# Performance work log

Hardware: AMD Instinct MI355X
Metric: run time of the kernel (lower is better)

The kernel has to match this reference:

```python
import jax, jax.numpy as jnp
import numpy as np

N_NODES = 65536
N_EDGES = 1048576
VOCAB = 50000
HIDDEN = 256
LAYERS = 3
NUM_GRAPHS = 64
NEG_SLOPE = 0.2  # PyG GATConv default LeakyReLU slope
EPS = 1e-16      # PyG softmax denominator epsilon


def setup_inputs() -> dict:
    key = jax.random.key(0)
    ks = jax.random.split(key, 12)
    s = 0.02
    nodes = jax.random.randint(ks[0], (N_NODES,), 0, VOCAB, dtype=jnp.int32)
    edge_index = jax.random.randint(ks[1], (2, N_EDGES), 0, N_NODES, dtype=jnp.int32)
    batch = jnp.sort(jax.random.randint(ks[2], (N_NODES,), 0, NUM_GRAPHS, dtype=jnp.int32))
    emb = jax.random.normal(ks[3], (VOCAB, HIDDEN), jnp.float32) * s
    Wg = jax.random.normal(ks[4], (LAYERS, HIDDEN, HIDDEN), jnp.float32) * s
    a_src = jax.random.normal(ks[5], (LAYERS, HIDDEN), jnp.float32) * s
    a_dst = jax.random.normal(ks[6], (LAYERS, HIDDEN), jnp.float32) * s
    bg = jnp.zeros((LAYERS, HIDDEN), jnp.float32)
    Wl = jax.random.normal(ks[7], (LAYERS, HIDDEN, HIDDEN), jnp.float32) * s
    bl = jnp.zeros((LAYERS, HIDDEN), jnp.float32)
    Wout = jax.random.normal(ks[8], (HIDDEN, VOCAB), jnp.float32) * s
    bout = jnp.zeros((VOCAB,), jnp.float32)
    return {"nodes": nodes, "edge_index": edge_index, "batch": batch,
            "emb": emb, "Wg": Wg, "a_src": a_src, "a_dst": a_dst, "bg": bg,
            "Wl": Wl, "bl": bl, "Wout": Wout, "bout": bout}


def _gat_layer(x, src, dst, W, a_s, a_d, b, n):
    h = x @ W                                    # [N, H]
    e = jax.nn.leaky_relu((h @ a_s)[src] + (h @ a_d)[dst], NEG_SLOPE)  # [E]
    m = jax.ops.segment_max(e, dst, num_segments=n)
    w = jnp.exp(e - m[dst])
    denom = jax.ops.segment_sum(w, dst, num_segments=n)
    alpha = w / (denom[dst] + EPS)               # segment softmax over incoming edges
    out = jax.ops.segment_sum(h[src] * alpha[:, None], dst, num_segments=n)
    return out + b


def reference(nodes, edge_index, batch, emb, Wg, a_src, a_dst, bg, Wl, bl, Wout, bout):
    n = nodes.shape[0]
    loop = jnp.arange(n, dtype=edge_index.dtype)  # GATConv add_self_loops=True
    src = jnp.concatenate([edge_index[0], loop])
    dst = jnp.concatenate([edge_index[1], loop])
    x = emb[nodes]                                # [N, H]
    for l in range(Wg.shape[0]):
        x = _gat_layer(x, src, dst, Wg[l], a_src[l], a_dst[l], bg[l], n)
        x = jax.nn.relu(x)
        x = x @ Wl[l] + bl[l]
    sums = jax.ops.segment_sum(x, batch, num_segments=NUM_GRAPHS)
    cnt = jax.ops.segment_sum(jnp.ones((n,), x.dtype), batch, num_segments=NUM_GRAPHS)
    pooled = sums / jnp.maximum(cnt, 1.0)[:, None]  # global mean pool -> [G, H]
    return pooled @ Wout + bout                      # [G, V]
```

## Files before the change

### kernel.cpp

```cpp
#include <hip/hip_runtime.h>

#define N_NODES 65536
#define N_EDGES 1048576
#define E_TOTAL (N_EDGES + N_NODES)
#define VOCAB 50000
#define HIDDEN 256
#define NUM_GRAPHS 64
#define NEG_SLOPE 0.2f
#define SM_EPS 1e-16f

#define NBKT 128
#define BKT_SHIFT 9
#define DSTS_PER_BKT 512
#define BKT_CAP 10240
#define EDGES_PER_BLK1 4352

typedef _Float16 f16x8 __attribute__((ext_vector_type(8)));
typedef _Float16 f16x4 __attribute__((ext_vector_type(4)));
typedef float f32x4 __attribute__((ext_vector_type(4)));

__global__ __launch_bounds__(256) void gather_kernel(const int* __restrict__ nodes,
    const float* __restrict__ emb, _Float16* __restrict__ x) {
    int i = blockIdx.x;
    int t = threadIdx.x;
    x[(size_t)i * HIDDEN + t] = (_Float16)emb[(size_t)nodes[i] * HIDDEN + t];
}

__global__ __launch_bounds__(256) void convert_wt_kernel(const float* __restrict__ Wg,
    _Float16* __restrict__ WT) {
    int n = blockIdx.x;
    int k = threadIdx.x;
    WT[(size_t)n * HIDDEN + k] = (_Float16)Wg[(size_t)k * HIDDEN + n];
}

__global__ __launch_bounds__(256) void fuse_w_kernel(const float* __restrict__ Wl,
    const float* __restrict__ Wg, _Float16* __restrict__ WT) {
    int pair = blockIdx.y;
    int n = blockIdx.x;
    int k = threadIdx.x;
    const float* A = Wl + (size_t)pair * HIDDEN * HIDDEN;
    const float* B = Wg + (size_t)(pair + 1) * HIDDEN * HIDDEN;
    float s = 0.f;
    for (int j = 0; j < HIDDEN; j++) s += A[(size_t)k * HIDDEN + j] * B[(size_t)j * HIDDEN + n];
    WT[(size_t)(1 + pair) * HIDDEN * HIDDEN + (size_t)n * HIDDEN + k] = (_Float16)s;
}

__global__ __launch_bounds__(256) void fuse_b_kernel(const float* __restrict__ Wg,
    const float* __restrict__ bl, float* __restrict__ bfused) {
    int pair = blockIdx.x;
    int n = threadIdx.x;
    const float* B = Wg + (size_t)(pair + 1) * HIDDEN * HIDDEN;
    const float* b = bl + (size_t)pair * HIDDEN;
    float s = 0.f;
    for (int k = 0; k < HIDDEN; k++) s += b[k] * B[(size_t)k * HIDDEN + n];
    bfused[pair * HIDDEN + n] = s;
}

__global__ __launch_bounds__(256) void bucket_kernel(const int* __restrict__ ei,
    int* __restrict__ bcur, unsigned* __restrict__ staging) {
    __shared__ int lhist[NBKT];
    __shared__ int lbase[NBKT];
    __shared__ int lcur[NBKT];
    int tid = threadIdx.x;
    if (tid < NBKT) lhist[tid] = 0;
    __syncthreads();
    int e0 = blockIdx.x * EDGES_PER_BLK1;
    int mySrc[17], myDst[17];
    #pragma unroll
    for (int k = 0; k < 17; k++) {
        int e = e0 + k * 256 + tid;
        int src, dst;
        if (e < N_EDGES) { src = ei[e]; dst = ei[N_EDGES + e]; }
        else             { src = dst = e - N_EDGES; }
        mySrc[k] = src; myDst[k] = dst;
        atomicAdd(&lhist[dst >> BKT_SHIFT], 1);
    }
    __syncthreads();
    if (tid < NBKT) {
        int c = lhist[tid];
        lbase[tid] = (c > 0) ? atomicAdd(&bcur[tid], c) : 0;
        lcur[tid] = 0;
    }
    __syncthreads();
    #pragma unroll
    for (int k = 0; k < 17; k++) {
        int b = myDst[k] >> BKT_SHIFT;
        int pos = lbase[b] + atomicAdd(&lcur[b], 1);
        staging[(size_t)b * BKT_CAP + pos] =
            ((unsigned)(myDst[k] & (DSTS_PER_BKT - 1)) << 16) | (unsigned)mySrc[k];
    }
}

__global__ __launch_bounds__(256) void csr_kernel(const int* __restrict__ bcur,
    const unsigned* __restrict__ staging, int* __restrict__ row_ptr,
    int* __restrict__ src_sorted) {
    __shared__ unsigned sedge[BKT_CAP];
    __shared__ int shist[DSTS_PER_BKT];
    __shared__ int sbase[DSTS_PER_BKT];
    __shared__ int spart[256];
    int b = blockIdx.x;
    int tid = threadIdx.x;
    int cnt = bcur[b];

    spart[tid] = (tid < NBKT && tid < b) ? bcur[tid] : 0;
    __syncthreads();
    for (int d = 128; d > 0; d >>= 1) {
        if (tid < d) spart[tid] += spart[tid + d];
        __syncthreads();
    }
    int base = spart[0];
    __syncthreads();

    shist[tid] = 0; shist[tid + 256] = 0;
    __syncthreads();
    for (int i = tid; i < cnt; i += 256) {
        unsigned v = staging[(size_t)b * BKT_CAP + i];
        sedge[i] = v;
        atomicAdd(&shist[v >> 16], 1);
    }
    __syncthreads();
    int p = shist[2 * tid] + shist[2 * tid + 1];
    spart[tid] = p;
    __syncthreads();
    for (int d = 1; d < 256; d <<= 1) {
        int v = (tid >= d) ? spart[tid - d] : 0;
        __syncthreads();
        spart[tid] += v;
        __syncthreads();
    }
    int epair = spart[tid] - p;
    sbase[2 * tid] = epair;
    sbase[2 * tid + 1] = epair + shist[2 * tid];
    __syncthreads();
    row_ptr[b * DSTS_PER_BKT + tid] = base + sbase[tid];
    row_ptr[b * DSTS_PER_BKT + 256 + tid] = base + sbase[256 + tid];
    shist[tid] = sbase[tid];
    shist[tid + 256] = sbase[tid + 256];
    __syncthreads();
    for (int i = tid; i < cnt; i += 256) {
        unsigned v = sedge[i];
        int d = v >> 16;
        int pos = atomicAdd(&shist[d], 1);
        src_sorted[base + pos] = (int)(v & 0xFFFFu);
    }
    if (b == NBKT - 1 && tid == 0) row_ptr[N_NODES] = E_TOTAL;
}

#define PAD_K 40
template <bool FUSED>
__global__ __launch_bounds__(256) void gemm_f16_kernel(const _Float16* __restrict__ A,
    const _Float16* __restrict__ WT, const float* __restrict__ bias,
    _Float16* __restrict__ C,
    const float* __restrict__ a_s, const float* __restrict__ a_d,
    float* __restrict__ es, float* __restrict__ ed) {
    __shared__ _Float16 As[128][PAD_K];
    __shared__ _Float16 Bs[128][PAD_K];
    int tid = threadIdx.x;
    int wave = tid >> 6;
    int lane = tid & 63;
    int quad = lane >> 4;
    int l16 = lane & 15;
    int m0 = blockIdx.x * 128;
    int n0 = blockIdx.y * 128;

    f32x4 acc[2][8];
    #pragma unroll
    for (int rt = 0; rt < 2; rt++)
        #pragma unroll
        for (int ct = 0; ct < 8; ct++)
            acc[rt][ct] = (f32x4){0.f, 0.f, 0.f, 0.f};

    for (int k0 = 0; k0 < HIDDEN; k0 += 32) {
        __syncthreads();
        #pragma unroll
        for (int i = 0; i < 2; i++) {
            int c = tid + i * 256;
            int row = c >> 2, q = c & 3;
            *(f16x8*)&As[row][q * 8] =
                *(const f16x8*)(A + (size_t)(m0 + row) * HIDDEN + k0 + q * 8);
        }
        #pragma unroll
        for (int i = 0; i < 2; i++) {
            int c = tid + i * 256;
            int row = c >> 2, q = c & 3;
            *(f16x8*)&Bs[row][q * 8] =
                *(const f16x8*)(WT + (size_t)(n0 + row) * HIDDEN + k0 + q * 8);
        }
        __syncthreads();
        f16x8 a0 = *(const f16x8*)&As[wave * 32 + l16][quad * 8];
        f16x8 a1 = *(const f16x8*)&As[wave * 32 + 16 + l16][quad * 8];
        #pragma unroll
        for (int ct = 0; ct < 8; ct++) {
            f16x8 b = *(const f16x8*)&Bs[ct * 16 + l16][quad * 8];
            acc[0][ct] = __builtin_amdgcn_mfma_f32_16x16x32_f16(a0, b, acc[0][ct], 0, 0, 0);
            acc[1][ct] = __builtin_amdgcn_mfma_f32_16x16x32_f16(a1, b, acc[1][ct], 0, 0, 0);
        }
    }
    #pragma unroll
    for (int rt = 0; rt < 2; rt++) {
        #pragma unroll
        for (int ct = 0; ct < 8; ct++) {
            int col = n0 + ct * 16 + l16;
            float bv = (bias != nullptr) ? bias[col] : 0.f;
            int rowbase = m0 + wave * 32 + rt * 16 + quad * 4;
            #pragma unroll
            for (int r = 0; r < 4; r++) {
                float hv = acc[rt][ct][r] + bv;
                acc[rt][ct][r] = hv;
                C[(size_t)(rowbase + r) * HIDDEN + col] = (_Float16)hv;
            }
        }
    }
    if (FUSED) {
        #pragma unroll
        for (int rt = 0; rt < 2; rt++) {
            float ds0 = 0.f, ds1 = 0.f, ds2 = 0.f, ds3 = 0.f;
            float dd0 = 0.f, dd1 = 0.f, dd2 = 0.f, dd3 = 0.f;
            #pragma unroll
            for (int ct = 0; ct < 8; ct++) {
                int col = n0 + ct * 16 + l16;
                float av = a_s[col];
                float dv = a_d[col];
                ds0 += acc[rt][ct][0] * av; dd0 += acc[rt][ct][0] * dv;
                ds1 += acc[rt][ct][1] * av; dd1 += acc[rt][ct][1] * dv;
                ds2 += acc[rt][ct][2] * av; dd2 += acc[rt][ct][2] * dv;
                ds3 += acc[rt][ct][3] * av; dd3 += acc[rt][ct][3] * dv;
            }
            #pragma unroll
            for (int off = 1; off < 16; off <<= 1) {
                ds0 += __shfl_xor(ds0, off); dd0 += __shfl_xor(dd0, off);
                ds1 += __shfl_xor(ds1, off); dd1 += __shfl_xor(dd1, off);
                ds2 += __shfl_xor(ds2, off); dd2 += __shfl_xor(dd2, off);
                ds3 += __shfl_xor(ds3, off); dd3 += __shfl_xor(dd3, off);
            }
            if (l16 == 0) {
                int rowbase = m0 + wave * 32 + rt * 16 + quad * 4;
                atomicAdd(&es[rowbase + 0], ds0); atomicAdd(&ed[rowbase + 0], dd0);
                atomicAdd(&es[rowbase + 1], ds1); atomicAdd(&ed[rowbase + 1], dd1);
                atomicAdd(&es[rowbase + 2], ds2); atomicAdd(&ed[rowbase + 2], dd2);
                atomicAdd(&es[rowbase + 3], ds3); atomicAdd(&ed[rowbase + 3], dd3);
            }
        }
    }
}

__global__ __launch_bounds__(256) void agg_kernel(const _Float16* __restrict__ h,
    const int* __restrict__ row_ptr, const int* __restrict__ src_sorted,
    const float* __restrict__ es, const float* __restrict__ ed,
    const float* __restrict__ bg, _Float16* __restrict__ g) {
    int dst = blockIdx.x * 8 + (threadIdx.x >> 5);
    int l32 = threadIdx.x & 31;
    int start = row_ptr[dst];
    int end = row_ptr[dst + 1];
    float edd = ed[dst];
    const _Float16* hl = h + l32 * 8;

    float den0 = 0.f, den1 = 0.f;
    float acc[8];
    #pragma unroll
    for (int j = 0; j < 8; j++) acc[j] = 0.f;

    int i = start;
    for (; i + 7 < end; i += 8) {
        int s0 = src_sorted[i + 0];
        int s1 = src_sorted[i + 1];
        int s2 = src_sorted[i + 2];
        int s3 = src_sorted[i + 3];
        int s4 = src_sorted[i + 4];
        int s5 = src_sorted[i + 5];
        int s6 = src_sorted[i + 6];
        int s7 = src_sorted[i + 7];
        f16x8 r0 = *(const f16x8*)(hl + (unsigned)s0 * HIDDEN);
        f16x8 r1 = *(const f16x8*)(hl + (unsigned)s1 * HIDDEN);
        f16x8 r2 = *(const f16x8*)(hl + (unsigned)s2 * HIDDEN);
        f16x8 r3 = *(const f16x8*)(hl + (unsigned)s3 * HIDDEN);
        f16x8 r4 = *(const f16x8*)(hl + (unsigned)s4 * HIDDEN);
        f16x8 r5 = *(const f16x8*)(hl + (unsigned)s5 * HIDDEN);
        f16x8 r6 = *(const f16x8*)(hl + (unsigned)s6 * HIDDEN);
        f16x8 r7 = *(const f16x8*)(hl + (unsigned)s7 * HIDDEN);
        float e0 = es[s0] + edd; e0 = (e0 > 0.f) ? e0 : NEG_SLOPE * e0;
        float e1 = es[s1] + edd; e1 = (e1 > 0.f) ? e1 : NEG_SLOPE * e1;
        float e2 = es[s2] + edd; e2 = (e2 > 0.f) ? e2 : NEG_SLOPE * e2;
        float e3 = es[s3] + edd; e3 = (e3 > 0.f) ? e3 : NEG_SLOPE * e3;
        float e4 = es[s4] + edd; e4 = (e4 > 0.f) ? e4 : NEG_SLOPE * e4;
        float e5 = es[s5] + edd; e5 = (e5 > 0.f) ? e5 : NEG_SLOPE * e5;
        float e6 = es[s6] + edd; e6 = (e6 > 0.f) ? e6 : NEG_SLOPE * e6;
        float e7 = es[s7] + edd; e7 = (e7 > 0.f) ? e7 : NEG_SLOPE * e7;
        float w0 = __expf(e0);
        float w1 = __expf(e1);
        float w2 = __expf(e2);
        float w3 = __expf(e3);
        float w4 = __expf(e4);
        float w5 = __expf(e5);
        float w6 = __expf(e6);
        float w7 = __expf(e7);
        den0 += (w0 + w1) + (w2 + w3);
        den1 += (w4 + w5) + (w6 + w7);
        #pragma unroll
        for (int j = 0; j < 8; j++)
            acc[j] += (w0 * (float)r0[j] + w1 * (float)r1[j])
                    + (w2 * (float)r2[j] + w3 * (float)r3[j])
                    + (w4 * (float)r4[j] + w5 * (float)r5[j])
                    + (w6 * (float)r6[j] + w7 * (float)r7[j]);
    }
    for (; i + 3 < end; i += 4) {
        int s0 = src_sorted[i + 0];
        int s1 = src_sorted[i + 1];
        int s2 = src_sorted[i + 2];
        int s3 = src_sorted[i + 3];
        f16x8 r0 = *(const f16x8*)(hl + (unsigned)s0 * HIDDEN);
        f16x8 r1 = *(const f16x8*)(hl + (unsigned)s1 * HIDDEN);
        f16x8 r2 = *(const f16x8*)(hl + (unsigned)s2 * HIDDEN);
        f16x8 r3 = *(const f16x8*)(hl + (unsigned)s3 * HIDDEN);
        float e0 = es[s0] + edd; e0 = (e0 > 0.f) ? e0 : NEG_SLOPE * e0;
        float e1 = es[s1] + edd; e1 = (e1 > 0.f) ? e1 : NEG_SLOPE * e1;
        float e2 = es[s2] + edd; e2 = (e2 > 0.f) ? e2 : NEG_SLOPE * e2;
        float e3 = es[s3] + edd; e3 = (e3 > 0.f) ? e3 : NEG_SLOPE * e3;
        float w0 = __expf(e0);
        float w1 = __expf(e1);
        float w2 = __expf(e2);
        float w3 = __expf(e3);
        den0 += (w0 + w1) + (w2 + w3);
        #pragma unroll
        for (int j = 0; j < 8; j++)
            acc[j] += (w0 * (float)r0[j] + w1 * (float)r1[j])
                    + (w2 * (float)r2[j] + w3 * (float)r3[j]);
    }
    for (; i < end; i++) {
        int s0 = src_sorted[i];
        f16x8 r0 = *(const f16x8*)(hl + (unsigned)s0 * HIDDEN);
        float e0 = es[s0] + edd; e0 = (e0 > 0.f) ? e0 : NEG_SLOPE * e0;
        float w0 = __expf(e0);
        den1 += w0;
        #pragma unroll
        for (int j = 0; j < 8; j++) acc[j] += w0 * (float)r0[j];
    }

    float inv = 1.0f / ((den0 + den1) + SM_EPS);
    float4 b0 = *(const float4*)(bg + l32 * 8);
    float4 b1 = *(const float4*)(bg + l32 * 8 + 4);
    f16x8 outv;
    outv[0] = (_Float16)fmaxf(acc[0] * inv + b0.x, 0.f);
    outv[1] = (_Float16)fmaxf(acc[1] * inv + b0.y, 0.f);
    outv[2] = (_Float16)fmaxf(acc[2] * inv + b0.z, 0.f);
    outv[3] = (_Float16)fmaxf(acc[3] * inv + b0.w, 0.f);
    outv[4] = (_Float16)fmaxf(acc[4] * inv + b1.x, 0.f);
    outv[5] = (_Float16)fmaxf(acc[5] * inv + b1.y, 0.f);
    outv[6] = (_Float16)fmaxf(acc[6] * inv + b1.z, 0.f);
    outv[7] = (_Float16)fmaxf(acc[7] * inv + b1.w, 0.f);
    *(f16x8*)(g + (size_t)dst * HIDDEN + l32 * 8) = outv;
}

__global__ __launch_bounds__(128) void graph_bounds_kernel(const int* __restrict__ batch,
    int* __restrict__ gstart) {
    int g = threadIdx.x;
    if (g > NUM_GRAPHS) return;
    if (g == NUM_GRAPHS) { gstart[NUM_GRAPHS] = N_NODES; return; }
    int lo = 0, hi = N_NODES;
    while (lo < hi) {
        int mid = (lo + hi) >> 1;
        if (batch[mid] < g) lo = mid + 1; else hi = mid;
    }
    gstart[g] = lo;
}

#define POOL_SPLITS 16
__global__ __launch_bounds__(256) void pool_partial_kernel(const _Float16* __restrict__ x,
    const int* __restrict__ gstart, float* __restrict__ pooledT) {
    int g = blockIdx.x;
    int chunk = blockIdx.y;
    int t = threadIdx.x;
    int s = gstart[g];
    int e = gstart[g + 1];
    int n = e - s;
    int per = (n + POOL_SPLITS - 1) / POOL_SPLITS;
    int r0 = s + chunk * per;
    int r1 = min(r0 + per, e);
    if (r0 >= r1) return;
    float acc = 0.f;
    for (int r = r0; r < r1; r++) acc += (float)x[(size_t)r * HIDDEN + t];
    atomicAdd(&pooledT[t * NUM_GRAPHS + g], acc);
}

__global__ __launch_bounds__(256) void mean_kernel(const float* __restrict__ pooledT,
    const int* __restrict__ gstart, float* __restrict__ meanT) {
    int i = blockIdx.x * 256 + threadIdx.x;
    int g = i & (NUM_GRAPHS - 1);
    float c = (float)max(gstart[g + 1] - gstart[g], 1);
    meanT[i] = pooledT[i] / c;
}

__global__ __launch_bounds__(256) void wl2_kernel(const float* __restrict__ meanP,
    const float* __restrict__ Wl, const float* __restrict__ bl,
    float* __restrict__ meanT2) {
    int g = blockIdx.x;
    int n = threadIdx.x;
    const float* W2 = Wl + (size_t)2 * HIDDEN * HIDDEN;
    float s = bl[2 * HIDDEN + n];
    for (int k = 0; k < HIDDEN; k++)
        s += meanP[k * NUM_GRAPHS + g] * W2[(size_t)k * HIDDEN + n];
    meanT2[n * NUM_GRAPHS + g] = s;
}

__global__ __launch_bounds__(256) void final_kernel(const float* __restrict__ meanT,
    const float* __restrict__ Wout, const float* __restrict__ bout, float* __restrict__ out) {
    int j = blockIdx.x * 64 + (threadIdx.x & 63);
    int g0 = __builtin_amdgcn_readfirstlane((threadIdx.x >> 6) * 16);
    if (j >= VOCAB) return;
    float acc[16];
    #pragma unroll
    for (int g = 0; g < 16; g++) acc[g] = 0.f;
    #pragma unroll 4
    for (int k = 0; k < HIDDEN; k++) {
        float w = Wout[(size_t)k * VOCAB + j];
        const float* mrow = meanT + k * NUM_GRAPHS + g0;
        #pragma unroll
        for (int g = 0; g < 16; g++) acc[g] += mrow[g] * w;
    }
    float b = bout[j];
    #pragma unroll
    for (int g = 0; g < 16; g++) out[(size_t)(g0 + g) * VOCAB + j] = acc[g] + b;
}

extern "C" void kernel_launch(void* const* d_in, const int* in_sizes, int n_in,
                              void* d_out, int out_size, void* d_ws, size_t ws_size,
                              hipStream_t stream) {
    const int*   nodes = (const int*)d_in[0];
    const int*   ei    = (const int*)d_in[1];
    const int*   batch = (const int*)d_in[2];
    const float* emb   = (const float*)d_in[3];
    const float* Wg    = (const float*)d_in[4];
    const float* a_src = (const float*)d_in[5];
    const float* a_dst = (const float*)d_in[6];
    const float* bg    = (const float*)d_in[7];
    const float* Wl    = (const float*)d_in[8];
    const float* bl    = (const float*)d_in[9];
    const float* Wout  = (const float*)d_in[10];
    const float* bout  = (const float*)d_in[11];
    float* out = (float*)d_out;

    char* ws = (char*)d_ws;
    size_t off = 0;
    auto alloc = [&](size_t bytes) -> void* {
        void* p = ws + off;
        off += (bytes + 255) & ~(size_t)255;
        return p;
    };
    _Float16* bufA    = (_Float16*)alloc((size_t)N_NODES * HIDDEN * 2);
    _Float16* bufB    = (_Float16*)alloc((size_t)N_NODES * HIDDEN * 2);
    _Float16* WT      = (_Float16*)alloc((size_t)3 * HIDDEN * HIDDEN * 2);
    float* bfused     = (float*)alloc((size_t)2 * HIDDEN * 4);
    float* es         = (float*)alloc((size_t)N_NODES * 4);
    float* ed         = (float*)alloc((size_t)N_NODES * 4);
    int*   row_ptr    = (int*)alloc((size_t)(N_NODES + 1) * 4);
    int*   src_sorted = (int*)alloc((size_t)E_TOTAL * 4);
    int*   bcur       = (int*)alloc((size_t)NBKT * 4);
    unsigned* staging = (unsigned*)alloc((size_t)NBKT * BKT_CAP * 4);
    float* pooledT    = (float*)alloc((size_t)HIDDEN * NUM_GRAPHS * 4);
    float* meanT      = (float*)alloc((size_t)HIDDEN * NUM_GRAPHS * 4);
    float* meanT2     = (float*)alloc((size_t)HIDDEN * NUM_GRAPHS * 4);
    int*   gstart     = (int*)alloc((size_t)(NUM_GRAPHS + 1) * 4);

    hipMemsetAsync(bcur, 0, (size_t)NBKT * 4, stream);
    hipMemsetAsync(pooledT, 0, (size_t)HIDDEN * NUM_GRAPHS * 4, stream);

    convert_wt_kernel<<<HIDDEN, 256, 0, stream>>>(Wg, WT);
    fuse_w_kernel<<<dim3(HIDDEN, 2), 256, 0, stream>>>(Wl, Wg, WT);
    fuse_b_kernel<<<2, 256, 0, stream>>>(Wg, bl, bfused);
    gather_kernel<<<N_NODES, 256, 0, stream>>>(nodes, emb, bufA);
    bucket_kernel<<<E_TOTAL / EDGES_PER_BLK1, 256, 0, stream>>>(ei, bcur, staging);
    csr_kernel<<<NBKT, 256, 0, stream>>>(bcur, staging, row_ptr, src_sorted);

    for (int l = 0; l < 3; l++) {
        hipMemsetAsync(es, 0, (size_t)N_NODES * 4, stream);
        hipMemsetAsync(ed, 0, (size_t)N_NODES * 4, stream);
        const float* bias = (l == 0) ? nullptr : (bfused + (size_t)(l - 1) * HIDDEN);
        gemm_f16_kernel<true><<<dim3(N_NODES / 128, 2), 256, 0, stream>>>(
            bufA, WT + (size_t)l * HIDDEN * HIDDEN, bias, bufB,
            a_src + (size_t)l * HIDDEN, a_dst + (size_t)l * HIDDEN, es, ed);
        agg_kernel<<<N_NODES / 8, 256, 0, stream>>>(
            bufB, row_ptr, src_sorted, es, ed, bg + (size_t)l * HIDDEN, bufA);
    }

    graph_bounds_kernel<<<1, 128, 0, stream>>>(batch, gstart);
    pool_partial_kernel<<<dim3(NUM_GRAPHS, POOL_SPLITS), 256, 0, stream>>>(bufA, gstart, pooledT);
    mean_kernel<<<(HIDDEN * NUM_GRAPHS) / 256, 256, 0, stream>>>(pooledT, gstart, meanT);
    wl2_kernel<<<NUM_GRAPHS, 256, 0, stream>>>(meanT, Wl, bl, meanT2);
    final_kernel<<<dim3((VOCAB + 63) / 64), 256, 0, stream>>>(meanT2, Wout, bout, out);
}
```

Measured before the change: 694.1 us.

## Sort destinations by degree for aggregation and replace atomics with partial-sum buffers

Measured after the change: 695.9 us. Within noise of the previous version (+0.3%).

```diff
diff --git a/kernel.cpp b/kernel.cpp
--- a/kernel.cpp
+++ b/kernel.cpp
@@ -14,6 +14,7 @@
 #define DSTS_PER_BKT 512
 #define BKT_CAP 10240
 #define EDGES_PER_BLK1 4352
+#define DEGBINS 128
 
 typedef _Float16 f16x8 __attribute__((ext_vector_type(8)));
 typedef _Float16 f16x4 __attribute__((ext_vector_type(4)));
@@ -146,13 +147,61 @@
     if (b == NBKT - 1 && tid == 0) row_ptr[N_NODES] = E_TOTAL;
 }
 
+__global__ __launch_bounds__(256) void deghist_kernel(const int* __restrict__ row_ptr,
+    int* __restrict__ dhist) {
+    __shared__ int lh[DEGBINS];
+    int tid = threadIdx.x;
+    if (tid < DEGBINS) lh[tid] = 0;
+    __syncthreads();
+    int d = blockIdx.x * 256 + tid;
+    int deg = min(row_ptr[d + 1] - row_ptr[d], DEGBINS - 1);
+    atomicAdd(&lh[deg], 1);
+    __syncthreads();
+    if (tid < DEGBINS && lh[tid]) atomicAdd(&dhist[tid], lh[tid]);
+}
+
+__global__ __launch_bounds__(128) void degscan_kernel(const int* __restrict__ dhist,
+    int* __restrict__ dbase) {
+    __shared__ int s[DEGBINS];
+    int t = threadIdx.x;
+    s[t] = dhist[t];
+    __syncthreads();
+    for (int d = 1; d < DEGBINS; d <<= 1) {
+        int v = (t >= d) ? s[t - d] : 0;
+        __syncthreads();
+        s[t] += v;
+        __syncthreads();
+    }
+    dbase[t] = s[t] - dhist[t];
+}
+
+__global__ __launch_bounds__(256) void degscatter_kernel(const int* __restrict__ row_ptr,
+    int* __restrict__ dbase, int* __restrict__ perm) {
+    __shared__ int lh[DEGBINS], lb[DEGBINS], lc[DEGBINS];
+    int tid = threadIdx.x;
+    if (tid < DEGBINS) lh[tid] = 0;
+    __syncthreads();
+    int d = blockIdx.x * 256 + tid;
+    int deg = min(row_ptr[d + 1] - row_ptr[d], DEGBINS - 1);
+    atomicAdd(&lh[deg], 1);
+    __syncthreads();
+    if (tid < DEGBINS) {
+        int c = lh[tid];
+        lb[tid] = c ? atomicAdd(&dbase[tid], c) : 0;
+        lc[tid] = 0;
+    }
+    __syncthreads();
+    int pos = lb[deg] + atomicAdd(&lc[deg], 1);
+    perm[pos] = d;
+}
+
 #define PAD_K 40
 template <bool FUSED>
 __global__ __launch_bounds__(256) void gemm_f16_kernel(const _Float16* __restrict__ A,
     const _Float16* __restrict__ WT, const float* __restrict__ bias,
     _Float16* __restrict__ C,
     const float* __restrict__ a_s, const float* __restrict__ a_d,
-    float* __restrict__ es, float* __restrict__ ed) {
+    float* __restrict__ esp, float* __restrict__ edp) {
     __shared__ _Float16 As[128][PAD_K];
     __shared__ _Float16 Bs[128][PAD_K];
     int tid = threadIdx.x;
@@ -212,6 +261,8 @@
         }
     }
     if (FUSED) {
+        float* esb = esp + (size_t)blockIdx.y * N_NODES;
+        float* edb = edp + (size_t)blockIdx.y * N_NODES;
         #pragma unroll
         for (int rt = 0; rt < 2; rt++) {
             float ds0 = 0.f, ds1 = 0.f, ds2 = 0.f, ds3 = 0.f;
@@ -235,20 +286,28 @@
             }
             if (l16 == 0) {
                 int rowbase = m0 + wave * 32 + rt * 16 + quad * 4;
-                atomicAdd(&es[rowbase + 0], ds0); atomicAdd(&ed[rowbase + 0], dd0);
-                atomicAdd(&es[rowbase + 1], ds1); atomicAdd(&ed[rowbase + 1], dd1);
-                atomicAdd(&es[rowbase + 2], ds2); atomicAdd(&ed[rowbase + 2], dd2);
-                atomicAdd(&es[rowbase + 3], ds3); atomicAdd(&ed[rowbase + 3], dd3);
+                esb[rowbase + 0] = ds0; edb[rowbase + 0] = dd0;
+                esb[rowbase + 1] = ds1; edb[rowbase + 1] = dd1;
+                esb[rowbase + 2] = ds2; edb[rowbase + 2] = dd2;
+                esb[rowbase + 3] = ds3; edb[rowbase + 3] = dd3;
             }
         }
     }
 }
 
+__global__ __launch_bounds__(256) void combine_kernel(const float* __restrict__ esp,
+    const float* __restrict__ edp, float* __restrict__ es, float* __restrict__ ed) {
+    int i = blockIdx.x * 256 + threadIdx.x;
+    es[i] = esp[i] + esp[N_NODES + i];
+    ed[i] = edp[i] + edp[N_NODES + i];
+}
+
 __global__ __launch_bounds__(256) void agg_kernel(const _Float16* __restrict__ h,
     const int* __restrict__ row_ptr, const int* __restrict__ src_sorted,
+    const int* __restrict__ perm,
     const float* __restrict__ es, const float* __restrict__ ed,
     const float* __restrict__ bg, _Float16* __restrict__ g) {
-    int dst = blockIdx.x * 8 + (threadIdx.x >> 5);
+    int dst = perm[blockIdx.x * 8 + (threadIdx.x >> 5)];
     int l32 = threadIdx.x & 31;
     int start = row_ptr[dst];
     int end = row_ptr[dst + 1];
@@ -450,11 +509,16 @@
     _Float16* bufB    = (_Float16*)alloc((size_t)N_NODES * HIDDEN * 2);
     _Float16* WT      = (_Float16*)alloc((size_t)3 * HIDDEN * HIDDEN * 2);
     float* bfused     = (float*)alloc((size_t)2 * HIDDEN * 4);
+    float* esp        = (float*)alloc((size_t)2 * N_NODES * 4);
+    float* edp        = (float*)alloc((size_t)2 * N_NODES * 4);
     float* es         = (float*)alloc((size_t)N_NODES * 4);
     float* ed         = (float*)alloc((size_t)N_NODES * 4);
     int*   row_ptr    = (int*)alloc((size_t)(N_NODES + 1) * 4);
     int*   src_sorted = (int*)alloc((size_t)E_TOTAL * 4);
+    int*   perm       = (int*)alloc((size_t)N_NODES * 4);
     int*   bcur       = (int*)alloc((size_t)NBKT * 4);
+    int*   dhist      = (int*)alloc((size_t)DEGBINS * 4);
+    int*   dbase      = (int*)alloc((size_t)DEGBINS * 4);
     unsigned* staging = (unsigned*)alloc((size_t)NBKT * BKT_CAP * 4);
     float* pooledT    = (float*)alloc((size_t)HIDDEN * NUM_GRAPHS * 4);
     float* meanT      = (float*)alloc((size_t)HIDDEN * NUM_GRAPHS * 4);
@@ -462,6 +526,7 @@
     int*   gstart     = (int*)alloc((size_t)(NUM_GRAPHS + 1) * 4);
 
     hipMemsetAsync(bcur, 0, (size_t)NBKT * 4, stream);
+    hipMemsetAsync(dhist, 0, (size_t)DEGBINS * 4, stream);
     hipMemsetAsync(pooledT, 0, (size_t)HIDDEN * NUM_GRAPHS * 4, stream);
 
     convert_wt_kernel<<<HIDDEN, 256, 0, stream>>>(Wg, WT);
@@ -470,16 +535,18 @@
     gather_kernel<<<N_NODES, 256, 0, stream>>>(nodes, emb, bufA);
     bucket_kernel<<<E_TOTAL / EDGES_PER_BLK1, 256, 0, stream>>>(ei, bcur, staging);
     csr_kernel<<<NBKT, 256, 0, stream>>>(bcur, staging, row_ptr, src_sorted);
+    deghist_kernel<<<N_NODES / 256, 256, 0, stream>>>(row_ptr, dhist);
+    degscan_kernel<<<1, DEGBINS, 0, stream>>>(dhist, dbase);
+    degscatter_kernel<<<N_NODES / 256, 256, 0, stream>>>(row_ptr, dbase, perm);
 
     for (int l = 0; l < 3; l++) {
-        hipMemsetAsync(es, 0, (size_t)N_NODES * 4, stream);
-        hipMemsetAsync(ed, 0, (size_t)N_NODES * 4, stream);
         const float* bias = (l == 0) ? nullptr : (bfused + (size_t)(l - 1) * HIDDEN);
         gemm_f16_kernel<true><<<dim3(N_NODES / 128, 2), 256, 0, stream>>>(
             bufA, WT + (size_t)l * HIDDEN * HIDDEN, bias, bufB,
-            a_src + (size_t)l * HIDDEN, a_dst + (size_t)l * HIDDEN, es, ed);
+            a_src + (size_t)l * HIDDEN, a_dst + (size_t)l * HIDDEN, esp, edp);
+        combine_kernel<<<N_NODES / 256, 256, 0, stream>>>(esp, edp, es, ed);
         agg_kernel<<<N_NODES / 8, 256, 0, stream>>>(
-            bufB, row_ptr, src_sorted, es, ed, bg + (size_t)l * HIDDEN, bufA);
+            bufB, row_ptr, src_sorted, perm, es, ed, bg + (size_t)l * HIDDEN, bufA);
     }
 
     graph_bounds_kernel<<<1, 128, 0, stream>>>(batch, gstart);
```

## Use full-width GEMM tiles so attention logits are stored without atomics

Applied to the files above, without the earlier changes.

After: 675.8 us. 2.6% less time.

```diff
diff --git a/kernel.cpp b/kernel.cpp
--- a/kernel.cpp
+++ b/kernel.cpp
@@ -26,23 +26,22 @@
     x[(size_t)i * HIDDEN + t] = (_Float16)emb[(size_t)nodes[i] * HIDDEN + t];
 }
 
-__global__ __launch_bounds__(256) void convert_wt_kernel(const float* __restrict__ Wg,
-    _Float16* __restrict__ WT) {
+__global__ __launch_bounds__(256) void prep_wt_kernel(const float* __restrict__ Wg,
+    const float* __restrict__ Wl, _Float16* __restrict__ WT) {
+    int mat = blockIdx.y;
     int n = blockIdx.x;
     int k = threadIdx.x;
-    WT[(size_t)n * HIDDEN + k] = (_Float16)Wg[(size_t)k * HIDDEN + n];
-}
-
-__global__ __launch_bounds__(256) void fuse_w_kernel(const float* __restrict__ Wl,
-    const float* __restrict__ Wg, _Float16* __restrict__ WT) {
-    int pair = blockIdx.y;
-    int n = blockIdx.x;
-    int k = threadIdx.x;
-    const float* A = Wl + (size_t)pair * HIDDEN * HIDDEN;
-    const float* B = Wg + (size_t)(pair + 1) * HIDDEN * HIDDEN;
-    float s = 0.f;
-    for (int j = 0; j < HIDDEN; j++) s += A[(size_t)k * HIDDEN + j] * B[(size_t)j * HIDDEN + n];
-    WT[(size_t)(1 + pair) * HIDDEN * HIDDEN + (size_t)n * HIDDEN + k] = (_Float16)s;
+    float s;
+    if (mat == 0) {
+        s = Wg[(size_t)k * HIDDEN + n];
+    } else {
+        const float* A = Wl + (size_t)(mat - 1) * HIDDEN * HIDDEN;
+        const float* B = Wg + (size_t)mat * HIDDEN * HIDDEN;
+        s = 0.f;
+        for (int j = 0; j < HIDDEN; j++)
+            s += A[(size_t)k * HIDDEN + j] * B[(size_t)j * HIDDEN + n];
+    }
+    WT[(size_t)mat * HIDDEN * HIDDEN + (size_t)n * HIDDEN + k] = (_Float16)s;
 }
 
 __global__ __launch_bounds__(256) void fuse_b_kernel(const float* __restrict__ Wg,
@@ -153,93 +152,78 @@
     _Float16* __restrict__ C,
     const float* __restrict__ a_s, const float* __restrict__ a_d,
     float* __restrict__ es, float* __restrict__ ed) {
-    __shared__ _Float16 As[128][PAD_K];
-    __shared__ _Float16 Bs[128][PAD_K];
+    __shared__ _Float16 As[64][PAD_K];
+    __shared__ _Float16 Bs[256][PAD_K];
     int tid = threadIdx.x;
     int wave = tid >> 6;
     int lane = tid & 63;
     int quad = lane >> 4;
     int l16 = lane & 15;
-    int m0 = blockIdx.x * 128;
-    int n0 = blockIdx.y * 128;
-
-    f32x4 acc[2][8];
-    #pragma unroll
-    for (int rt = 0; rt < 2; rt++)
-        #pragma unroll
-        for (int ct = 0; ct < 8; ct++)
-            acc[rt][ct] = (f32x4){0.f, 0.f, 0.f, 0.f};
+    int m0 = blockIdx.x * 64;
+
+    f32x4 acc[16];
+    #pragma unroll
+    for (int ct = 0; ct < 16; ct++) acc[ct] = (f32x4){0.f, 0.f, 0.f, 0.f};
 
     for (int k0 = 0; k0 < HIDDEN; k0 += 32) {
         __syncthreads();
-        #pragma unroll
-        for (int i = 0; i < 2; i++) {
-            int c = tid + i * 256;
-            int row = c >> 2, q = c & 3;
+        {
+            int row = tid >> 2, q = tid & 3;
             *(f16x8*)&As[row][q * 8] =
                 *(const f16x8*)(A + (size_t)(m0 + row) * HIDDEN + k0 + q * 8);
         }
         #pragma unroll
-        for (int i = 0; i < 2; i++) {
+        for (int i = 0; i < 4; i++) {
             int c = tid + i * 256;
             int row = c >> 2, q = c & 3;
             *(f16x8*)&Bs[row][q * 8] =
-                *(const f16x8*)(WT + (size_t)(n0 + row) * HIDDEN + k0 + q * 8);
+                *(const f16x8*)(WT + (size_t)row * HIDDEN + k0 + q * 8);
         }
         __syncthreads();
-        f16x8 a0 = *(const f16x8*)&As[wave * 32 + l16][quad * 8];
-        f16x8 a1 = *(const f16x8*)&As[wave * 32 + 16 + l16][quad * 8];
-        #pragma unroll
-        for (int ct = 0; ct < 8; ct++) {
+        f16x8 a = *(const f16x8*)&As[wave * 16 + l16][quad * 8];
+        #pragma unroll
+        for (int ct = 0; ct < 16; ct++) {
             f16x8 b = *(const f16x8*)&Bs[ct * 16 + l16][quad * 8];
-            acc[0][ct] = __builtin_amdgcn_mfma_f32_16x16x32_f16(a0, b, acc[0][ct], 0, 0, 0);
-            acc[1][ct] = __builtin_amdgcn_mfma_f32_16x16x32_f16(a1, b, acc[1][ct], 0, 0, 0);
-        }
-    }
-    #pragma unroll
-    for (int rt = 0; rt < 2; rt++) {
-        #pragma unroll
-        for (int ct = 0; ct < 8; ct++) {
-            int col = n0 + ct * 16 + l16;
-            float bv = (bias != nullptr) ? bias[col] : 0.f;
-            int rowbase = m0 + wave * 32 + rt * 16 + quad * 4;
-            #pragma unroll
-            for (int r = 0; r < 4; r++) {
-                float hv = acc[rt][ct][r] + bv;
-                acc[rt][ct][r] = hv;
-                C[(size_t)(rowbase + r) * HIDDEN + col] = (_Float16)hv;
-            }
+            acc[ct] = __builtin_amdgcn_mfma_f32_16x16x32_f16(a, b, acc[ct], 0, 0, 0);
+        }
+    }
+    int rowbase = m0 + wave * 16 + quad * 4;
+    #pragma unroll
+    for (int ct = 0; ct < 16; ct++) {
+        int col = ct * 16 + l16;
+        float bv = (bias != nullptr) ? bias[col] : 0.f;
+        #pragma unroll
+        for (int r = 0; r < 4; r++) {
+            float hv = acc[ct][r] + bv;
+            acc[ct][r] = hv;
+            C[(size_t)(rowbase + r) * HIDDEN + col] = (_Float16)hv;
         }
     }
     if (FUSED) {
-        #pragma unroll
-        for (int rt = 0; rt < 2; rt++) {
-            float ds0 = 0.f, ds1 = 0.f, ds2 = 0.f, ds3 = 0.f;
-            float dd0 = 0.f, dd1 = 0.f, dd2 = 0.f, dd3 = 0.f;
-            #pragma unroll
-            for (int ct = 0; ct < 8; ct++) {
-                int col = n0 + ct * 16 + l16;
-                float av = a_s[col];
-                float dv = a_d[col];
-                ds0 += acc[rt][ct][0] * av; dd0 += acc[rt][ct][0] * dv;
-                ds1 += acc[rt][ct][1] * av; dd1 += acc[rt][ct][1] * dv;
-                ds2 += acc[rt][ct][2] * av; dd2 += acc[rt][ct][2] * dv;
-                ds3 += acc[rt][ct][3] * av; dd3 += acc[rt][ct][3] * dv;
-            }
-            #pragma unroll
-            for (int off = 1; off < 16; off <<= 1) {
-                ds0 += __shfl_xor(ds0, off); dd0 += __shfl_xor(dd0, off);
-                ds1 += __shfl_xor(ds1, off); dd1 += __shfl_xor(dd1, off);
-                ds2 += __shfl_xor(ds2, off); dd2 += __shfl_xor(dd2, off);
-                ds3 += __shfl_xor(ds3, off); dd3 += __shfl_xor(dd3, off);
-            }
-            if (l16 == 0) {
-                int rowbase = m0 + wave * 32 + rt * 16 + quad * 4;
-                atomicAdd(&es[rowbase + 0], ds0); atomicAdd(&ed[rowbase + 0], dd0);
-                atomicAdd(&es[rowbase + 1], ds1); atomicAdd(&ed[rowbase + 1], dd1);
-                atomicAdd(&es[rowbase + 2], ds2); atomicAdd(&ed[rowbase + 2], dd2);
-                atomicAdd(&es[rowbase + 3], ds3); atomicAdd(&ed[rowbase + 3], dd3);
-            }
+        float ds0 = 0.f, ds1 = 0.f, ds2 = 0.f, ds3 = 0.f;
+        float dd0 = 0.f, dd1 = 0.f, dd2 = 0.f, dd3 = 0.f;
+        #pragma unroll
+        for (int ct = 0; ct < 16; ct++) {
+            int col = ct * 16 + l16;
+            float av = a_s[col];
+            float dv = a_d[col];
+            ds0 += acc[ct][0] * av; dd0 += acc[ct][0] * dv;
+            ds1 += acc[ct][1] * av; dd1 += acc[ct][1] * dv;
+            ds2 += acc[ct][2] * av; dd2 += acc[ct][2] * dv;
+            ds3 += acc[ct][3] * av; dd3 += acc[ct][3] * dv;
+        }
+        #pragma unroll
+        for (int off = 1; off < 16; off <<= 1) {
+            ds0 += __shfl_xor(ds0, off); dd0 += __shfl_xor(dd0, off);
+            ds1 += __shfl_xor(ds1, off); dd1 += __shfl_xor(dd1, off);
+            ds2 += __shfl_xor(ds2, off); dd2 += __shfl_xor(dd2, off);
+            ds3 += __shfl_xor(ds3, off); dd3 += __shfl_xor(dd3, off);
+        }
+        if (l16 == 0) {
+            es[rowbase + 0] = ds0; ed[rowbase + 0] = dd0;
+            es[rowbase + 1] = ds1; ed[rowbase + 1] = dd1;
+            es[rowbase + 2] = ds2; ed[rowbase + 2] = dd2;
+            es[rowbase + 3] = ds3; ed[rowbase + 3] = dd3;
         }
     }
 }
@@ -464,18 +448,15 @@
     hipMemsetAsync(bcur, 0, (size_t)NBKT * 4, stream);
     hipMemsetAsync(pooledT, 0, (size_t)HIDDEN * NUM_GRAPHS * 4, stream);
 
-    convert_wt_kernel<<<HIDDEN, 256, 0, stream>>>(Wg, WT);
-    fuse_w_kernel<<<dim3(HIDDEN, 2), 256, 0, stream>>>(Wl, Wg, WT);
+    prep_wt_kernel<<<dim3(HIDDEN, 3), 256, 0, stream>>>(Wg, Wl, WT);
     fuse_b_kernel<<<2, 256, 0, stream>>>(Wg, bl, bfused);
     gather_kernel<<<N_NODES, 256, 0, stream>>>(nodes, emb, bufA);
     bucket_kernel<<<E_TOTAL / EDGES_PER_BLK1, 256, 0, stream>>>(ei, bcur, staging);
     csr_kernel<<<NBKT, 256, 0, stream>>>(bcur, staging, row_ptr, src_sorted);
 
     for (int l = 0; l < 3; l++) {
-        hipMemsetAsync(es, 0, (size_t)N_NODES * 4, stream);
-        hipMemsetAsync(ed, 0, (size_t)N_NODES * 4, stream);
         const float* bias = (l == 0) ? nullptr : (bfused + (size_t)(l - 1) * HIDDEN);
-        gemm_f16_kernel<true><<<dim3(N_NODES / 128, 2), 256, 0, stream>>>(
+        gemm_f16_kernel<true><<<N_NODES / 64, 256, 0, stream>>>(
             bufA, WT + (size_t)l * HIDDEN * HIDDEN, bias, bufB,
             a_src + (size_t)l * HIDDEN, a_dst + (size_t)l * HIDDEN, es, ed);
         agg_kernel<<<N_NODES / 8, 256, 0, stream>>>(
```
